# Performance work log

Hardware: AMD Instinct MI355X
Metric: run time of the kernel (lower is better)

## Reference

```python
import jax, jax.numpy as jnp
import numpy as np


def _lin_lrelu(x, W, b):
    # LinearBlock(c_in, c_out): Linear + LeakyReLU(0.01)
    return jax.nn.leaky_relu(x @ W + b)


def _mrconv(x_src, x_dst, edges, index_id, W, b):
    """BipartiteResMRConv: gather-diff-scatter_max + residual MLP.
    x_src: [B, Ns, C], x_dst: [B, Nd, C], edges: [2, E] int."""
    src = index_id[0][edges[0]]                     # [E]
    dst = index_id[0][edges[1]]                     # [E]
    diffs = x_dst[:, dst, :] - x_src[:, src, :]     # [B, E, C]
    d = jnp.swapaxes(diffs, 0, 1)                   # [E, B, C] (segment axis leading)
    m = jax.ops.segment_max(d, dst, num_segments=x_dst.shape[1])  # [Nd, B, C]
    m = jnp.where(jnp.isneginf(m), 0.0, m)          # empty segments -> 0 (maxes init zeros)
    maxes = jnp.swapaxes(m, 0, 1)                   # [B, Nd, C]
    h = jnp.concatenate([x_dst, maxes], axis=2)     # [B, Nd, 2C]
    return x_dst + _lin_lrelu(h, W, b)


def setup_inputs() -> dict:
    key = jax.random.key(0)
    ks = jax.random.split(key, 24)
    B, Nf, Ne, Nv, C = 4, 40000, 80000, 40000, 32
    E_fe, E_ev, E_ff, E_ef, E_ve = 160000, 160000, 240000, 160000, 160000

    def edges(k, E, ns, nd):
        k1, k2 = jax.random.split(k)
        return jnp.stack([jax.random.randint(k1, (E,), 0, ns),
                          jax.random.randint(k2, (E,), 0, nd)]).astype(jnp.int64)

    inp = {
        "x_f": jax.random.normal(ks[0], (B, Nf, 4), jnp.float32),
        "x_e": jax.random.normal(ks[1], (B, Ne, 6), jnp.float32),
        "x_v": jax.random.normal(ks[2], (B, Nv, 3), jnp.float32),
        "index_id": jnp.arange(max(Nf, Ne, Nv), dtype=jnp.int64)[None, :],
        "fe_edges": edges(ks[3], E_fe, Nf, Ne),
        "ev_edges": edges(ks[4], E_ev, Ne, Nv),
        "ff_edges": edges(ks[5], E_ff, Nf, Nf),
        "ef_edges": edges(ks[6], E_ef, Ne, Nf),
        "ve_edges": edges(ks[7], E_ve, Nv, Ne),
        "Wf": jax.random.normal(ks[8], (4, C), jnp.float32) * 0.1,
        "bf": jnp.zeros((C,), jnp.float32),
        "We": jax.random.normal(ks[9], (6, C), jnp.float32) * 0.1,
        "be": jnp.zeros((C,), jnp.float32),
        "Wv": jax.random.normal(ks[10], (3, C), jnp.float32) * 0.1,
        "bv": jnp.zeros((C,), jnp.float32),
    }
    for i, name in enumerate(["f2e", "e2v", "ff", "e2f", "v2e"]):
        inp[f"W_{name}"] = jax.random.normal(ks[11 + i], (2 * C, C), jnp.float32) * 0.1
        inp[f"b_{name}"] = jnp.zeros((C,), jnp.float32)
    return inp


def reference(x_f, x_e, x_v, index_id, fe_edges, ev_edges, ff_edges, ef_edges,
              ve_edges, Wf, bf, We, be, Wv, bv, W_f2e, b_f2e, W_e2v, b_e2v,
              W_ff, b_ff, W_e2f, b_e2f, W_v2e, b_v2e):
    xf0 = _lin_lrelu(x_f, Wf, bf)   # [B, Nf, 32]
    xe0 = _lin_lrelu(x_e, We, be)   # [B, Ne, 32]
    xv0 = _lin_lrelu(x_v, Wv, bv)   # [B, Nv, 32]
    xe = _mrconv(xf0, xe0, fe_edges, index_id, W_f2e, b_f2e)   # F2E
    xv = _mrconv(xe0, xv0, ev_edges, index_id, W_e2v, b_e2v)   # E2V
    xf = _mrconv(xf0, xf0, ff_edges, index_id, W_ff, b_ff)     # F2F (ffLayers)
    xf = _mrconv(xe, xf, ef_edges, index_id, W_e2f, b_e2f)     # E2F
    xe = _mrconv(xv, xe, ve_edges, index_id, W_v2e, b_v2e)     # V2E
    return (xf, xe, xv)
```

## Files before the change

kernel.cpp:

```cpp
#include <hip/hip_runtime.h>
#include <float.h>

#define LRELU(v) ((v) > 0.0f ? (v) : 0.01f * (v))

__device__ __forceinline__ int f2ord(float f) {
    int i = __float_as_int(f);
    return (i >= 0) ? i : (int)(0x80000000u - (unsigned int)i);
}
__device__ __forceinline__ float ord2f(int m) {
    int i = (m >= 0) ? m : (int)(0x80000000u - (unsigned int)m);
    return __int_as_float(i);
}

__global__ void prep(const float* __restrict__ xf, const float* __restrict__ xe,
                     const float* __restrict__ xv,
                     const float* __restrict__ Wf, const float* __restrict__ bf,
                     const float* __restrict__ We, const float* __restrict__ be,
                     const float* __restrict__ Wv, const float* __restrict__ bv,
                     float* __restrict__ of, float* __restrict__ oe,
                     float* __restrict__ ov,
                     const int* __restrict__ e0, const int* __restrict__ e1,
                     const int* __restrict__ e2, const int* __restrict__ e3,
                     const int* __restrict__ e4, int* __restrict__ cur,
                     int* __restrict__ slots) {
    int bid = blockIdx.x;
    int t = threadIdx.x;
    if (bid < 20000) {
        int loc = bid * 256 + t;
        const int QF = 1280000, QE = 2560000;
        const float* x; const float* W; const float* bb; float* o; int cin;
        if (loc < QF)           { x = xf; W = Wf; bb = bf; o = of; cin = 4; }
        else if (loc < QF + QE) { x = xe; W = We; bb = be; o = oe; cin = 6; loc -= QF; }
        else                    { x = xv; W = Wv; bb = bv; o = ov; cin = 3; loc -= QF + QE; }
        int c0 = (loc & 7) * 4;
        int r  = loc >> 3;
        float4 acc = *(const float4*)(bb + c0);
        for (int k = 0; k < cin; ++k) {
            float xv_ = x[r * cin + k];
            float4 wv = *(const float4*)(W + k * 32 + c0);
            acc.x = fmaf(xv_, wv.x, acc.x); acc.y = fmaf(xv_, wv.y, acc.y);
            acc.z = fmaf(xv_, wv.z, acc.z); acc.w = fmaf(xv_, wv.w, acc.w);
        }
        float4 ov4;
        ov4.x = LRELU(acc.x); ov4.y = LRELU(acc.y);
        ov4.z = LRELU(acc.z); ov4.w = LRELU(acc.w);
        ((float4*)o)[loc] = ov4;
    } else {
        int idx = (bid - 20000) * 256 + t;
        if (idx >= 880000) return;
        const int cum[6]  = {0, 160000, 320000, 560000, 720000, 880000};
        const int bOff[5] = {0, 2500, 3750, 5000, 6250};
        const int Eg[5]   = {160000, 160000, 240000, 160000, 160000};
        const int* eds[5] = {e0, e1, e2, e3, e4};
        int g = 0;
#pragma unroll
        for (int k = 1; k < 5; ++k) g += (idx >= cum[k]);
        int e = idx - cum[g];
        int s = eds[g][e];
        int d = eds[g][Eg[g] + e];
        int cbase = (bOff[g] + (d >> 5)) * 8 + (idx & 7);
        int c = atomicAdd(&cur[cbase], 1);
        if (c < 64) slots[(size_t)cbase * 64 + c] = (s << 5) | (d & 31);
    }
}

struct ConvJob {
    const float* xsrc; const float* xdst;
    const int* cur; const int* slots;
    const float* W; const float* bias; float* out;
    int Ns; int Nd; int blkStart;
};
struct ConvJobs { ConvJob e[3]; };

__global__ __launch_bounds__(256, 1)
void conv_fused(ConvJobs jobs) {
    __shared__ int smxi[128][33];
    int t = threadIdx.x;
    int bid = blockIdx.x;
    int g = (bid >= jobs.e[2].blkStart) ? 2 : (bid >= jobs.e[1].blkStart) ? 1 : 0;
    const float* xsrc  = jobs.e[g].xsrc;
    const float* xdst  = jobs.e[g].xdst;
    const int*   cur   = jobs.e[g].cur;
    const int*   slots = jobs.e[g].slots;
    const float* W     = jobs.e[g].W;
    const float* bias  = jobs.e[g].bias;
    float*       out   = jobs.e[g].out;
    int Ns = jobs.e[g].Ns, Nd = jobs.e[g].Nd;
    int lb = bid - jobs.e[g].blkStart;
    int base = lb * 32;

    for (int i = t; i < 128 * 33; i += 256) ((int*)smxi)[i] = 0x7FFFFFFF;
    __syncthreads();

    int w    = t >> 6;
    int lane = t & 63;
    int r    = (w & 1) * 64 + lane;
    int c0   = __builtin_amdgcn_readfirstlane((w >> 1) * 16);
    int nl = r >> 2, b2 = r & 3;
    int d  = base + nl;
    const float* xdp = xdst + ((size_t)b2 * Nd + d) * 32;
    float xd[32];
#pragma unroll
    for (int q = 0; q < 8; ++q) {
        float4 v = ((const float4*)xdp)[q];
        xd[4*q] = v.x; xd[4*q+1] = v.y; xd[4*q+2] = v.z; xd[4*q+3] = v.w;
    }

    {
        int c4 = t & 7;
        int b  = (t >> 3) & 3;
        int el = t >> 5;
        int len = cur[lb * 8 + el];
        len = len > 64 ? 64 : len;
        const int* ce = slots + (size_t)(lb * 8 + el) * 64;
        const float* xsb = xsrc + (size_t)b * Ns * 32 + c4 * 4;
        for (int j = 0; j < len; j += 8) {
            int4 sw0 = *(const int4*)(ce + j);
            int4 sw1 = *(const int4*)(ce + j + 4);
            int sea = sw0.x;
            int se1 = (j + 1 < len) ? sw0.y : sea;
            int se2 = (j + 2 < len) ? sw0.z : sea;
            int se3 = (j + 3 < len) ? sw0.w : sea;
            int se4 = (j + 4 < len) ? sw1.x : sea;
            int se5 = (j + 5 < len) ? sw1.y : sea;
            int se6 = (j + 6 < len) ? sw1.z : sea;
            int se7 = (j + 7 < len) ? sw1.w : sea;
            float4 v0 = *(const float4*)(xsb + (size_t)(sea >> 5) * 32);
            float4 v1 = *(const float4*)(xsb + (size_t)(se1 >> 5) * 32);
            float4 v2 = *(const float4*)(xsb + (size_t)(se2 >> 5) * 32);
            float4 v3 = *(const float4*)(xsb + (size_t)(se3 >> 5) * 32);
            float4 v4 = *(const float4*)(xsb + (size_t)(se4 >> 5) * 32);
            float4 v5 = *(const float4*)(xsb + (size_t)(se5 >> 5) * 32);
            float4 v6 = *(const float4*)(xsb + (size_t)(se6 >> 5) * 32);
            float4 v7 = *(const float4*)(xsb + (size_t)(se7 >> 5) * 32);
#define MINGRP(se, v)  { int* mr = &smxi[((se) & 31) * 4 + b][c4 * 4]; \
            atomicMin(&mr[0], f2ord((v).x)); atomicMin(&mr[1], f2ord((v).y)); \
            atomicMin(&mr[2], f2ord((v).z)); atomicMin(&mr[3], f2ord((v).w)); }
            MINGRP(sea, v0) MINGRP(se1, v1) MINGRP(se2, v2) MINGRP(se3, v3)
            MINGRP(se4, v4) MINGRP(se5, v5) MINGRP(se6, v6) MINGRP(se7, v7)
#undef MINGRP
        }
    }
    __syncthreads();

    bool has = (smxi[r][0] != 0x7FFFFFFF);
    float mx[32];
#pragma unroll
    for (int q = 0; q < 32; ++q) {
        int iv = smxi[r][q];
        mx[q] = has ? (xd[q] - ord2f(iv)) : 0.0f;
    }
    const float* Wc = W + c0;
    float acc[16];
#pragma unroll
    for (int jj = 0; jj < 16; ++jj) acc[jj] = bias[c0 + jj];
#pragma unroll
    for (int k = 0; k < 64; ++k) {
        float hk = (k < 32) ? xd[k] : mx[k - 32];
        const float4* wr = (const float4*)(Wc + k * 32);
        float4 w0 = wr[0], w1 = wr[1], w2 = wr[2], w3 = wr[3];
        acc[0]  = fmaf(hk, w0.x, acc[0]);  acc[1]  = fmaf(hk, w0.y, acc[1]);
        acc[2]  = fmaf(hk, w0.z, acc[2]);  acc[3]  = fmaf(hk, w0.w, acc[3]);
        acc[4]  = fmaf(hk, w1.x, acc[4]);  acc[5]  = fmaf(hk, w1.y, acc[5]);
        acc[6]  = fmaf(hk, w1.z, acc[6]);  acc[7]  = fmaf(hk, w1.w, acc[7]);
        acc[8]  = fmaf(hk, w2.x, acc[8]);  acc[9]  = fmaf(hk, w2.y, acc[9]);
        acc[10] = fmaf(hk, w2.z, acc[10]); acc[11] = fmaf(hk, w2.w, acc[11]);
        acc[12] = fmaf(hk, w3.x, acc[12]); acc[13] = fmaf(hk, w3.y, acc[13]);
        acc[14] = fmaf(hk, w3.z, acc[14]); acc[15] = fmaf(hk, w3.w, acc[15]);
    }
    float xr[16];
#pragma unroll
    for (int i = 0; i < 16; ++i) xr[i] = (c0 == 0) ? xd[i] : xd[16 + i];
    float* op = out + ((size_t)b2 * Nd + d) * 32 + c0;
#pragma unroll
    for (int q = 0; q < 4; ++q) {
        float4 o;
        float a0 = acc[4*q], a1 = acc[4*q+1], a2 = acc[4*q+2], a3 = acc[4*q+3];
        o.x = xr[4*q]   + LRELU(a0); o.y = xr[4*q+1] + LRELU(a1);
        o.z = xr[4*q+2] + LRELU(a2); o.w = xr[4*q+3] + LRELU(a3);
        ((float4*)op)[q] = o;
    }
}

extern "C" void kernel_launch(void* const* d_in, const int* in_sizes, int n_in,
                              void* d_out, int out_size, void* d_ws, size_t ws_size,
                              hipStream_t stream) {
    const float* x_f = (const float*)d_in[0];
    const float* x_e = (const float*)d_in[1];
    const float* x_v = (const float*)d_in[2];
    const int* fe = (const int*)d_in[4];
    const int* ev = (const int*)d_in[5];
    const int* ff = (const int*)d_in[6];
    const int* ef = (const int*)d_in[7];
    const int* ve = (const int*)d_in[8];
    const float* Wf = (const float*)d_in[9];
    const float* bf = (const float*)d_in[10];
    const float* We = (const float*)d_in[11];
    const float* be = (const float*)d_in[12];
    const float* Wv = (const float*)d_in[13];
    const float* bv = (const float*)d_in[14];
    const float* W_f2e = (const float*)d_in[15];
    const float* b_f2e = (const float*)d_in[16];
    const float* W_e2v = (const float*)d_in[17];
    const float* b_e2v = (const float*)d_in[18];
    const float* W_ff  = (const float*)d_in[19];
    const float* b_ff  = (const float*)d_in[20];
    const float* W_e2f = (const float*)d_in[21];
    const float* b_e2f = (const float*)d_in[22];
    const float* W_v2e = (const float*)d_in[23];
    const float* b_v2e = (const float*)d_in[24];

    const int B = 4, Nf = 40000, Ne = 80000, Nv = 40000;
    const int NFC = B * Nf * 32;
    const int NEC = B * Ne * 32;
    const int NVC = B * Nv * 32;
    const int CUR_TOTAL = 70016;
    const int SLOT_TOTAL = 8750 * 512;
    const int INT_WORDS = CUR_TOTAL + SLOT_TOTAL;

    float* oxf = (float*)d_out;
    float* oxe = oxf + NFC;
    float* oxv = oxe + NEC;

    size_t needA = (size_t)(NFC + 2 * NEC) * 4 + (size_t)INT_WORDS * 4;
    bool merged = ws_size >= needA;

    float* ws  = (float*)d_ws;
    float* xf0 = ws;
    float* xe0 = ws + NFC;
    float* xe1 = merged ? (ws + NFC + NEC) : oxe;
    int* cur   = (int*)(merged ? (ws + NFC + 2 * NEC) : (ws + NFC + NEC));
    int* slots = cur + CUR_TOTAL;

    hipMemsetAsync(cur, 0, (size_t)CUR_TOTAL * 4, stream);

    prep<<<20000 + 3438, 256, 0, stream>>>(
        x_f, x_e, x_v, Wf, bf, We, be, Wv, bv, xf0, xe0, oxv,
        fe, ev, ff, ef, ve, cur, slots);

    const int* cu_f2e = cur;            const int* sl_f2e = slots;
    const int* cu_e2v = cur + 2500*8;   const int* sl_e2v = slots + (size_t)2500*512;
    const int* cu_ff  = cur + 3750*8;   const int* sl_ff  = slots + (size_t)3750*512;
    const int* cu_e2f = cur + 5000*8;   const int* sl_e2f = slots + (size_t)5000*512;
    const int* cu_v2e = cur + 6250*8;   const int* sl_v2e = slots + (size_t)6250*512;

    {
        ConvJobs j;
        j.e[0] = {xf0, xe0, cu_f2e, sl_f2e, W_f2e, b_f2e, xe1, Nf, Ne, 0};
        j.e[1] = {xe0, oxv, cu_e2v, sl_e2v, W_e2v, b_e2v, oxv, Ne, Nv, 2500};
        j.e[2] = {xf0, xf0, cu_ff,  sl_ff,  W_ff,  b_ff,  oxf, Nf, Nf, 3750};
        conv_fused<<<5000, 256, 0, stream>>>(j);
    }
    if (merged) {
        ConvJobs j;
        j.e[0] = {xe1, oxf, cu_e2f, sl_e2f, W_e2f, b_e2f, oxf, Ne, Nf, 0};
        j.e[1] = {oxv, xe1, cu_v2e, sl_v2e, W_v2e, b_v2e, oxe, Nv, Ne, 1250};
        j.e[2] = j.e[0]; j.e[2].blkStart = 0x7FFFFFFF;
        conv_fused<<<3750, 256, 0, stream>>>(j);
    } else {
        {
            ConvJobs j;
            j.e[0] = {oxe, oxf, cu_e2f, sl_e2f, W_e2f, b_e2f, oxf, Ne, Nf, 0};
            j.e[1] = j.e[0]; j.e[1].blkStart = 0x7FFFFFFF;
            j.e[2] = j.e[0]; j.e[2].blkStart = 0x7FFFFFFF;
            conv_fused<<<1250, 256, 0, stream>>>(j);
        }
        {
            ConvJobs j;
            j.e[0] = {oxv, oxe, cu_v2e, sl_v2e, W_v2e, b_v2e, oxe, Nv, Ne, 0};
            j.e[1] = j.e[0]; j.e[1].blkStart = 0x7FFFFFFF;
            j.e[2] = j.e[0]; j.e[2].blkStart = 0x7FFFFFFF;
            conv_fused<<<2500, 256, 0, stream>>>(j);
        }
    }
}
```

Measured before the change: 378.4 us.

## Fuse vertex input linear into E2V conv and unroll gather loop by sixteen

The vertex input LinearBlock (3->32 with LeakyReLU) is no longer run in prep. The E2V conv job now computes it on the fly from raw x_v when loading destination features, which removes a full write and read of the xv0 intermediate and shrinks the prep grid. The neighbor gather loop is unrolled from 8 to 16 slots so more loads are in flight, and the source offset is computed with a mask instead of a shift-multiply. The unroll raises register pressure, and the fused path adds a runtime cin branch plus per-thread loads of the weights.

```diff
diff --git a/kernel.cpp b/kernel.cpp
--- a/kernel.cpp
+++ b/kernel.cpp
@@ -13,25 +13,21 @@
 }
 
 __global__ void prep(const float* __restrict__ xf, const float* __restrict__ xe,
-                     const float* __restrict__ xv,
                      const float* __restrict__ Wf, const float* __restrict__ bf,
                      const float* __restrict__ We, const float* __restrict__ be,
-                     const float* __restrict__ Wv, const float* __restrict__ bv,
                      float* __restrict__ of, float* __restrict__ oe,
-                     float* __restrict__ ov,
                      const int* __restrict__ e0, const int* __restrict__ e1,
                      const int* __restrict__ e2, const int* __restrict__ e3,
                      const int* __restrict__ e4, int* __restrict__ cur,
                      int* __restrict__ slots) {
     int bid = blockIdx.x;
     int t = threadIdx.x;
-    if (bid < 20000) {
+    if (bid < 15000) {
         int loc = bid * 256 + t;
-        const int QF = 1280000, QE = 2560000;
+        const int QF = 1280000;
         const float* x; const float* W; const float* bb; float* o; int cin;
-        if (loc < QF)           { x = xf; W = Wf; bb = bf; o = of; cin = 4; }
-        else if (loc < QF + QE) { x = xe; W = We; bb = be; o = oe; cin = 6; loc -= QF; }
-        else                    { x = xv; W = Wv; bb = bv; o = ov; cin = 3; loc -= QF + QE; }
+        if (loc < QF) { x = xf; W = Wf; bb = bf; o = of; cin = 4; }
+        else          { x = xe; W = We; bb = be; o = oe; cin = 6; loc -= QF; }
         int c0 = (loc & 7) * 4;
         int r  = loc >> 3;
         float4 acc = *(const float4*)(bb + c0);
@@ -46,7 +42,7 @@
         ov4.z = LRELU(acc.z); ov4.w = LRELU(acc.w);
         ((float4*)o)[loc] = ov4;
     } else {
-        int idx = (bid - 20000) * 256 + t;
+        int idx = (bid - 15000) * 256 + t;
         if (idx >= 880000) return;
         const int cum[6]  = {0, 160000, 320000, 560000, 720000, 880000};
         const int bOff[5] = {0, 2500, 3750, 5000, 6250};
@@ -68,7 +64,8 @@
     const float* xsrc; const float* xdst;
     const int* cur; const int* slots;
     const float* W; const float* bias; float* out;
-    int Ns; int Nd; int blkStart;
+    const float* xraw; const float* Wlin; const float* blin;
+    int Ns; int Nd; int blkStart; int cin;
 };
 struct ConvJobs { ConvJob e[3]; };
 
@@ -85,7 +82,11 @@
     const float* W     = jobs.e[g].W;
     const float* bias  = jobs.e[g].bias;
     float*       out   = jobs.e[g].out;
+    const float* xraw  = jobs.e[g].xraw;
+    const float* Wlin  = jobs.e[g].Wlin;
+    const float* blin  = jobs.e[g].blin;
     int Ns = jobs.e[g].Ns, Nd = jobs.e[g].Nd;
+    int cin = jobs.e[g].cin;
     int lb = bid - jobs.e[g].blkStart;
     int base = lb * 32;
 
@@ -98,12 +99,26 @@
     int c0   = __builtin_amdgcn_readfirstlane((w >> 1) * 16);
     int nl = r >> 2, b2 = r & 3;
     int d  = base + nl;
-    const float* xdp = xdst + ((size_t)b2 * Nd + d) * 32;
     float xd[32];
-#pragma unroll
-    for (int q = 0; q < 8; ++q) {
-        float4 v = ((const float4*)xdp)[q];
-        xd[4*q] = v.x; xd[4*q+1] = v.y; xd[4*q+2] = v.z; xd[4*q+3] = v.w;
+    if (cin > 0) {
+#pragma unroll
+        for (int c = 0; c < 32; ++c) xd[c] = blin[c];
+        const float* xrp = xraw + ((size_t)b2 * Nd + d) * cin;
+        for (int k = 0; k < cin; ++k) {
+            float xrk = xrp[k];
+            const float* wk = Wlin + k * 32;
+#pragma unroll
+            for (int c = 0; c < 32; ++c) xd[c] = fmaf(xrk, wk[c], xd[c]);
+        }
+#pragma unroll
+        for (int c = 0; c < 32; ++c) xd[c] = LRELU(xd[c]);
+    } else {
+        const float* xdp = xdst + ((size_t)b2 * Nd + d) * 32;
+#pragma unroll
+        for (int q = 0; q < 8; ++q) {
+            float4 v = ((const float4*)xdp)[q];
+            xd[4*q] = v.x; xd[4*q+1] = v.y; xd[4*q+2] = v.z; xd[4*q+3] = v.w;
+        }
     }
 
     {
@@ -114,30 +129,50 @@
         len = len > 64 ? 64 : len;
         const int* ce = slots + (size_t)(lb * 8 + el) * 64;
         const float* xsb = xsrc + (size_t)b * Ns * 32 + c4 * 4;
-        for (int j = 0; j < len; j += 8) {
+        for (int j = 0; j < len; j += 16) {
             int4 sw0 = *(const int4*)(ce + j);
             int4 sw1 = *(const int4*)(ce + j + 4);
-            int sea = sw0.x;
-            int se1 = (j + 1 < len) ? sw0.y : sea;
-            int se2 = (j + 2 < len) ? sw0.z : sea;
-            int se3 = (j + 3 < len) ? sw0.w : sea;
-            int se4 = (j + 4 < len) ? sw1.x : sea;
-            int se5 = (j + 5 < len) ? sw1.y : sea;
-            int se6 = (j + 6 < len) ? sw1.z : sea;
-            int se7 = (j + 7 < len) ? sw1.w : sea;
-            float4 v0 = *(const float4*)(xsb + (size_t)(sea >> 5) * 32);
-            float4 v1 = *(const float4*)(xsb + (size_t)(se1 >> 5) * 32);
-            float4 v2 = *(const float4*)(xsb + (size_t)(se2 >> 5) * 32);
-            float4 v3 = *(const float4*)(xsb + (size_t)(se3 >> 5) * 32);
-            float4 v4 = *(const float4*)(xsb + (size_t)(se4 >> 5) * 32);
-            float4 v5 = *(const float4*)(xsb + (size_t)(se5 >> 5) * 32);
-            float4 v6 = *(const float4*)(xsb + (size_t)(se6 >> 5) * 32);
-            float4 v7 = *(const float4*)(xsb + (size_t)(se7 >> 5) * 32);
+            int4 sw2 = *(const int4*)(ce + j + 8);
+            int4 sw3 = *(const int4*)(ce + j + 12);
+            int sea  = sw0.x;
+            int se1  = (j + 1  < len) ? sw0.y : sea;
+            int se2  = (j + 2  < len) ? sw0.z : sea;
+            int se3  = (j + 3  < len) ? sw0.w : sea;
+            int se4  = (j + 4  < len) ? sw1.x : sea;
+            int se5  = (j + 5  < len) ? sw1.y : sea;
+            int se6  = (j + 6  < len) ? sw1.z : sea;
+            int se7  = (j + 7  < len) ? sw1.w : sea;
+            int se8  = (j + 8  < len) ? sw2.x : sea;
+            int se9  = (j + 9  < len) ? sw2.y : sea;
+            int se10 = (j + 10 < len) ? sw2.z : sea;
+            int se11 = (j + 11 < len) ? sw2.w : sea;
+            int se12 = (j + 12 < len) ? sw3.x : sea;
+            int se13 = (j + 13 < len) ? sw3.y : sea;
+            int se14 = (j + 14 < len) ? sw3.z : sea;
+            int se15 = (j + 15 < len) ? sw3.w : sea;
+            float4 v0  = *(const float4*)(xsb + (size_t)(sea  & ~31));
+            float4 v1  = *(const float4*)(xsb + (size_t)(se1  & ~31));
+            float4 v2  = *(const float4*)(xsb + (size_t)(se2  & ~31));
+            float4 v3  = *(const float4*)(xsb + (size_t)(se3  & ~31));
+            float4 v4  = *(const float4*)(xsb + (size_t)(se4  & ~31));
+            float4 v5  = *(const float4*)(xsb + (size_t)(se5  & ~31));
+            float4 v6  = *(const float4*)(xsb + (size_t)(se6  & ~31));
+            float4 v7  = *(const float4*)(xsb + (size_t)(se7  & ~31));
+            float4 v8  = *(const float4*)(xsb + (size_t)(se8  & ~31));
+            float4 v9  = *(const float4*)(xsb + (size_t)(se9  & ~31));
+            float4 v10 = *(const float4*)(xsb + (size_t)(se10 & ~31));
+            float4 v11 = *(const float4*)(xsb + (size_t)(se11 & ~31));
+            float4 v12 = *(const float4*)(xsb + (size_t)(se12 & ~31));
+            float4 v13 = *(const float4*)(xsb + (size_t)(se13 & ~31));
+            float4 v14 = *(const float4*)(xsb + (size_t)(se14 & ~31));
+            float4 v15 = *(const float4*)(xsb + (size_t)(se15 & ~31));
 #define MINGRP(se, v)  { int* mr = &smxi[((se) & 31) * 4 + b][c4 * 4]; \
             atomicMin(&mr[0], f2ord((v).x)); atomicMin(&mr[1], f2ord((v).y)); \
             atomicMin(&mr[2], f2ord((v).z)); atomicMin(&mr[3], f2ord((v).w)); }
-            MINGRP(sea, v0) MINGRP(se1, v1) MINGRP(se2, v2) MINGRP(se3, v3)
-            MINGRP(se4, v4) MINGRP(se5, v5) MINGRP(se6, v6) MINGRP(se7, v7)
+            MINGRP(sea,  v0)  MINGRP(se1,  v1)  MINGRP(se2,  v2)  MINGRP(se3,  v3)
+            MINGRP(se4,  v4)  MINGRP(se5,  v5)  MINGRP(se6,  v6)  MINGRP(se7,  v7)
+            MINGRP(se8,  v8)  MINGRP(se9,  v9)  MINGRP(se10, v10) MINGRP(se11, v11)
+            MINGRP(se12, v12) MINGRP(se13, v13) MINGRP(se14, v14) MINGRP(se15, v15)
 #undef MINGRP
         }
     }
@@ -213,7 +248,6 @@
     const int B = 4, Nf = 40000, Ne = 80000, Nv = 40000;
     const int NFC = B * Nf * 32;
     const int NEC = B * Ne * 32;
-    const int NVC = B * Nv * 32;
     const int CUR_TOTAL = 70016;
     const int SLOT_TOTAL = 8750 * 512;
     const int INT_WORDS = CUR_TOTAL + SLOT_TOTAL;
@@ -234,8 +268,8 @@
 
     hipMemsetAsync(cur, 0, (size_t)CUR_TOTAL * 4, stream);
 
-    prep<<<20000 + 3438, 256, 0, stream>>>(
-        x_f, x_e, x_v, Wf, bf, We, be, Wv, bv, xf0, xe0, oxv,
+    prep<<<15000 + 3438, 256, 0, stream>>>(
+        x_f, x_e, Wf, bf, We, be, xf0, xe0,
         fe, ev, ff, ef, ve, cur, slots);
 
     const int* cu_f2e = cur;            const int* sl_f2e = slots;
@@ -246,28 +280,35 @@
 
     {
         ConvJobs j;
-        j.e[0] = {xf0, xe0, cu_f2e, sl_f2e, W_f2e, b_f2e, xe1, Nf, Ne, 0};
-        j.e[1] = {xe0, oxv, cu_e2v, sl_e2v, W_e2v, b_e2v, oxv, Ne, Nv, 2500};
-        j.e[2] = {xf0, xf0, cu_ff,  sl_ff,  W_ff,  b_ff,  oxf, Nf, Nf, 3750};
+        j.e[0] = {xf0, xe0, cu_f2e, sl_f2e, W_f2e, b_f2e, xe1,
+                  nullptr, nullptr, nullptr, Nf, Ne, 0, 0};
+        j.e[1] = {xe0, oxv, cu_e2v, sl_e2v, W_e2v, b_e2v, oxv,
+                  x_v, Wv, bv, Ne, Nv, 2500, 3};
+        j.e[2] = {xf0, xf0, cu_ff,  sl_ff,  W_ff,  b_ff,  oxf,
+                  nullptr, nullptr, nullptr, Nf, Nf, 3750, 0};
         conv_fused<<<5000, 256, 0, stream>>>(j);
     }
     if (merged) {
         ConvJobs j;
-        j.e[0] = {xe1, oxf, cu_e2f, sl_e2f, W_e2f, b_e2f, oxf, Ne, Nf, 0};
-        j.e[1] = {oxv, xe1, cu_v2e, sl_v2e, W_v2e, b_v2e, oxe, Nv, Ne, 1250};
+        j.e[0] = {xe1, oxf, cu_e2f, sl_e2f, W_e2f, b_e2f, oxf,
+                  nullptr, nullptr, nullptr, Ne, Nf, 0, 0};
+        j.e[1] = {oxv, xe1, cu_v2e, sl_v2e, W_v2e, b_v2e, oxe,
+                  nullptr, nullptr, nullptr, Nv, Ne, 1250, 0};
         j.e[2] = j.e[0]; j.e[2].blkStart = 0x7FFFFFFF;
         conv_fused<<<3750, 256, 0, stream>>>(j);
     } else {
         {
             ConvJobs j;
-            j.e[0] = {oxe, oxf, cu_e2f, sl_e2f, W_e2f, b_e2f, oxf, Ne, Nf, 0};
+            j.e[0] = {oxe, oxf, cu_e2f, sl_e2f, W_e2f, b_e2f, oxf,
+                      nullptr, nullptr, nullptr, Ne, Nf, 0, 0};
             j.e[1] = j.e[0]; j.e[1].blkStart = 0x7FFFFFFF;
             j.e[2] = j.e[0]; j.e[2].blkStart = 0x7FFFFFFF;
             conv_fused<<<1250, 256, 0, stream>>>(j);
         }
         {
             ConvJobs j;
-            j.e[0] = {oxv, oxe, cu_v2e, sl_v2e, W_v2e, b_v2e, oxe, Nv, Ne, 0};
+            j.e[0] = {oxv, oxe, cu_v2e, sl_v2e, W_v2e, b_v2e, oxe,
+                      nullptr, nullptr, nullptr, Nv, Ne, 0, 0};
             j.e[1] = j.e[0]; j.e[1].blkStart = 0x7FFFFFFF;
             j.e[2] = j.e[0]; j.e[2].blkStart = 0x7FFFFFFF;
             conv_fused<<<2500, 256, 0, stream>>>(j);
```

Measured after the change: 400.8 us. 1.06x slower.
